# Kernel tuning notes

Measured on AMD Instinct MI355X. Metric: run time of the kernel, lower is better.

The kernel has to match this reference:

```python
import jax, jax.numpy as jnp
import numpy as np

B, T, DIM = 2, 2048, 2048
N_HEADS, N_KV_HEADS = 16, 4
HEAD_DIM = DIM // N_HEADS  # 128
N_REP = N_HEADS // N_KV_HEADS  # 4
ROPE_THETA = 10000.0


def setup_inputs() -> dict:
    key = jax.random.key(0)
    ks = jax.random.split(key, 5)
    x = jax.random.normal(ks[0], (B, T, DIM), dtype=jnp.float32)
    # RoPE tables (equivalent to complex freqs_cis = exp(i * t * inv_freq))
    inv_freq = 1.0 / (ROPE_THETA ** (np.arange(0, HEAD_DIM, 2, dtype=np.float32) / HEAD_DIM))
    t = np.arange(T, dtype=np.float32)
    ang = np.outer(t, inv_freq)  # (T, HEAD_DIM//2)
    freqs_cos = jnp.asarray(np.cos(ang), dtype=jnp.float32)
    freqs_sin = jnp.asarray(np.sin(ang), dtype=jnp.float32)
    s = 0.02
    wq = jax.random.normal(ks[1], (DIM, N_HEADS * HEAD_DIM), dtype=jnp.float32) * s
    wk = jax.random.normal(ks[2], (DIM, N_KV_HEADS * HEAD_DIM), dtype=jnp.float32) * s
    wv = jax.random.normal(ks[3], (DIM, N_KV_HEADS * HEAD_DIM), dtype=jnp.float32) * s
    wo = jax.random.normal(ks[4], (N_HEADS * HEAD_DIM, DIM), dtype=jnp.float32) * s
    return {"x": x, "freqs_cos": freqs_cos, "freqs_sin": freqs_sin,
            "wq": wq, "wk": wk, "wv": wv, "wo": wo}


def _apply_rope(t, cos, sin):
    # t: (B, H, T, hd); cos/sin: (T, hd//2); interleaved pairs like view_as_complex
    tr = t[..., 0::2]
    ti = t[..., 1::2]
    c = cos[None, None, :, :]
    s = sin[None, None, :, :]
    out_r = tr * c - ti * s
    out_i = tr * s + ti * c
    return jnp.stack([out_r, out_i], axis=-1).reshape(t.shape)


def reference(x, freqs_cos, freqs_sin, wq, wk, wv, wo):
    Bb, Tt, C = x.shape
    q = (x @ wq).reshape(Bb, Tt, N_HEADS, HEAD_DIM).transpose(0, 2, 1, 3)      # (B,H,T,hd)
    k = (x @ wk).reshape(Bb, Tt, N_KV_HEADS, HEAD_DIM).transpose(0, 2, 1, 3)   # (B,KV,T,hd)
    v = (x @ wv).reshape(Bb, Tt, N_KV_HEADS, HEAD_DIM).transpose(0, 2, 1, 3)
    q = _apply_rope(q, freqs_cos[:Tt], freqs_sin[:Tt])
    k = _apply_rope(k, freqs_cos[:Tt], freqs_sin[:Tt])
    # GQA repeat_kv
    k = jnp.repeat(k, N_REP, axis=1)  # (B,H,T,hd)
    v = jnp.repeat(v, N_REP, axis=1)
    scale = 1.0 / jnp.sqrt(jnp.float32(HEAD_DIM))
    scores = jnp.einsum("bhqd,bhkd->bhqk", q, k) * scale
    causal = jnp.tril(jnp.ones((Tt, Tt), dtype=bool))
    scores = jnp.where(causal[None, None], scores, jnp.float32(-jnp.inf))
    attn = jax.nn.softmax(scores, axis=-1)
    out = jnp.einsum("bhqk,bhkd->bhqd", attn, v)          # (B,H,T,hd)
    out = out.transpose(0, 2, 1, 3).reshape(Bb, Tt, C)
    return out @ wo
```

## Files before the change

kernel.cpp:

```cpp
#include <hip/hip_runtime.h>
#include <hip/hip_bf16.h>

#define SEQT 2048
#define NH 16
#define HD 128

typedef __bf16 bf16;
typedef __bf16 bf16x4 __attribute__((ext_vector_type(4)));
typedef __bf16 bf16x8 __attribute__((ext_vector_type(8)));
typedef float f32x4 __attribute__((ext_vector_type(4)));
typedef float f32x16 __attribute__((ext_vector_type(16)));

__device__ inline void glds16(const bf16* g, bf16* l) {
  __builtin_amdgcn_global_load_lds(
      (const __attribute__((address_space(1))) unsigned int*)g,
      (__attribute__((address_space(3))) unsigned int*)l, 16, 0, 0);
}

__device__ inline unsigned int cvtpk(float a, float b) {
  unsigned int d;
  asm("v_cvt_pk_bf16_f32 %0, %1, %2" : "=v"(d) : "v"(a), "v"(b));
  return d;
}

__global__ __launch_bounds__(256) void k_convert(const float* __restrict__ in,
                                                 bf16* __restrict__ out, int n8) {
  int i = blockIdx.x * 256 + threadIdx.x;
  if (i >= n8) return;
  const float4* p = (const float4*)in + (size_t)i * 2;
  float4 a = p[0], b = p[1];
  bf16x8 o;
  o[0] = (bf16)a.x; o[1] = (bf16)a.y; o[2] = (bf16)a.z; o[3] = (bf16)a.w;
  o[4] = (bf16)b.x; o[5] = (bf16)b.y; o[6] = (bf16)b.z; o[7] = (bf16)b.w;
  *((bf16x8*)out + i) = o;
}

__global__ __launch_bounds__(256) void k_transpose(const float* __restrict__ in,
                                                   bf16* __restrict__ out, int R, int C) {
  __shared__ float tile[32][33];
  int c0 = blockIdx.x * 32, r0 = blockIdx.y * 32;
  int tx = threadIdx.x, ty = threadIdx.y;
#pragma unroll
  for (int i = 0; i < 4; i++)
    tile[ty + i * 8][tx] = in[(size_t)(r0 + ty + i * 8) * C + c0 + tx];
  __syncthreads();
#pragma unroll
  for (int i = 0; i < 4; i++) {
    int r = ty + i * 8;
    out[(size_t)(c0 + r) * R + r0 + tx] = (bf16)tile[tx][r];
  }
}

template <typename OutT>
__global__ __launch_bounds__(256) void k_gemm(const bf16* __restrict__ A,
                                              const bf16* __restrict__ Bt,
                                              OutT* __restrict__ C,
                                              int M, int N, int K, int ldc) {
  __shared__ bf16 Al[128 * 32];
  __shared__ bf16 Bl[128 * 32];
  int tid = threadIdx.x;
  int m0 = blockIdx.y * 128, n0 = blockIdx.x * 128;
  int wid = tid >> 6, lane = tid & 63;
  int wr = (wid >> 1) * 64, wc = (wid & 1) * 64;
  int lr = lane & 15, lk = (lane >> 4) * 8;
  f32x4 acc[4][4] = {};

  for (int k0 = 0; k0 < K; k0 += 32) {
#pragma unroll
    for (int i = 0; i < 2; i++) {
      int idx = i * 256 + tid;
      int r = idx >> 2, kc = (idx & 3) * 8;
      glds16(A + (size_t)(m0 + r) * K + k0 + kc, Al + idx * 8);
      glds16(Bt + (size_t)(n0 + r) * K + k0 + kc, Bl + idx * 8);
    }
    __syncthreads();
    bf16x8 af[4], bfr[4];
#pragma unroll
    for (int mi = 0; mi < 4; mi++) af[mi] = *(const bf16x8*)&Al[(wr + mi * 16 + lr) * 32 + lk];
#pragma unroll
    for (int ni = 0; ni < 4; ni++) bfr[ni] = *(const bf16x8*)&Bl[(wc + ni * 16 + lr) * 32 + lk];
#pragma unroll
    for (int mi = 0; mi < 4; mi++)
#pragma unroll
      for (int ni = 0; ni < 4; ni++)
        acc[mi][ni] = __builtin_amdgcn_mfma_f32_16x16x32_bf16(af[mi], bfr[ni], acc[mi][ni], 0, 0, 0);
    __syncthreads();
  }

  int rbase = m0 + wr + ((lane >> 4) << 2);
#pragma unroll
  for (int mi = 0; mi < 4; mi++)
#pragma unroll
    for (int ni = 0; ni < 4; ni++)
#pragma unroll
      for (int r = 0; r < 4; r++) {
        int row = rbase + mi * 16 + r;
        int col = n0 + wc + ni * 16 + lr;
        C[(size_t)row * ldc + col] = (OutT)acc[mi][ni][r];
      }
}

__global__ __launch_bounds__(256) void k_rope(bf16* __restrict__ qkv,
                                              const float* __restrict__ fcos,
                                              const float* __restrict__ fsin) {
  int gid = blockIdx.x * 256 + threadIdx.x;
  int row = gid / 1280;
  int p = gid % 1280;
  int head = p >> 6;
  int dp = p & 63;
  int t = row & (SEQT - 1);
  int colbase = head < NH ? head * HD : NH * HD + (head - NH) * HD;
  bf16* ptr = qkv + (size_t)row * 3072 + colbase + dp * 2;
  float a = (float)ptr[0], b = (float)ptr[1];
  float c = fcos[t * 64 + dp], s = fsin[t * 64 + dp];
  ptr[0] = (bf16)(a * c - b * s);
  ptr[1] = (bf16)(a * s + b * c);
}

__global__ __launch_bounds__(256, 2) void k_attn(const bf16* __restrict__ qkv,
                                                 bf16* __restrict__ attout) {
  __shared__ bf16 Kl[2][8192];
  __shared__ bf16 Vt[2][128][72];
  __shared__ float Tabs[4][4][32];
  int bid = blockIdx.x;
  int qt = 31 - (bid >> 5);
  int bh = bid & 31;
  int b = bh >> 4, h = bh & 15, kvh = h >> 2;
  int tid = threadIdx.x, wid = tid >> 6, lane = tid & 63;
  int grp = wid >> 1, wq = wid & 1;
  int li = lane & 31, hi = lane >> 5;
  int q0 = qt * 64;
  int qmin = q0 + wq * 32, qmax = qmin + 31;
  int qlane = qmin + li;
  const float C1 = 0.12751744979927212f;

  const bf16* kgbase = qkv + (size_t)b * SEQT * 3072 + 2048 + kvh * HD;
  const bf16* vgbase = kgbase + 512;

  bf16x8 qf[8];
  {
    const bf16* qb = qkv + (size_t)(b * SEQT + qlane) * 3072 + h * HD + hi * 8;
#pragma unroll
    for (int ks = 0; ks < 8; ks++) qf[ks] = *(const bf16x8*)(qb + ks * 16);
  }

  float mrun = -INFINITY, lpart = 0.f;
  f32x16 o0 = {}, o1 = {}, o2 = {}, o3 = {};
  int nkt = qt + 1;

  int g = (lane >> 4) & 3;
  int lr = lane & 15;
  int kq4 = (wid * 4 + g) * 4;
  int dc = lr * 8;
  int xr = (lr & 7) << 3;
  int kvw = kq4 ^ xr;

  bf16x8 vr0, vr1, vr2, vr3;

#pragma unroll
  for (int r = 0; r < 4; r++) {
    int ci = r * 256 + tid;
    int row = ci >> 4;
    int sl = (ci & 15) ^ (row & 15);
    glds16(kgbase + (size_t)row * 3072 + sl * 8, &Kl[0][ci * 8]);
  }
  {
    const bf16* vrow = vgbase + (size_t)kq4 * 3072 + dc;
    vr0 = *(const bf16x8*)(vrow);
    vr1 = *(const bf16x8*)(vrow + 3072);
    vr2 = *(const bf16x8*)(vrow + 6144);
    vr3 = *(const bf16x8*)(vrow + 9216);
  }

  for (int kt = 0; kt < nkt; kt++) {
    int cur = kt & 1;
    int kv0 = kt * 64;
    asm volatile("s_waitcnt vmcnt(0)" ::: "memory");

#pragma unroll
    for (int j = 0; j < 8; j++) {
      bf16x4 w;
      w[0] = vr0[j]; w[1] = vr1[j]; w[2] = vr2[j]; w[3] = vr3[j];
      *(bf16x4*)&Vt[cur][dc + j][kvw] = w;
    }

    asm volatile("s_waitcnt lgkmcnt(0)" ::: "memory");
    __builtin_amdgcn_sched_barrier(0);
    __builtin_amdgcn_s_barrier();
    __builtin_amdgcn_sched_barrier(0);

    if (kt + 1 < nkt) {
      int kv1 = kv0 + 64;
      bf16* kdst = &Kl[cur ^ 1][0];
#pragma unroll
      for (int r = 0; r < 4; r++) {
        int ci = r * 256 + tid;
        int row = ci >> 4;
        int sl = (ci & 15) ^ (row & 15);
        glds16(kgbase + (size_t)(kv1 + row) * 3072 + sl * 8, kdst + ci * 8);
      }
      const bf16* vrow = vgbase + (size_t)(kv1 + kq4) * 3072 + dc;
      vr0 = *(const bf16x8*)(vrow);
      vr1 = *(const bf16x8*)(vrow + 3072);
      vr2 = *(const bf16x8*)(vrow + 6144);
      vr3 = *(const bf16x8*)(vrow + 9216);
    }

    if (grp == cur && kv0 <= qmax) {
      f32x16 s0 = {}, s1 = {};
      const char* kb0 = (const char*)&Kl[cur][0] + li * 256;
      __builtin_amdgcn_s_setprio(1);
#pragma unroll
      for (int ks = 0; ks < 8; ks++) {
        int off = ((ks * 2 + hi) ^ (li & 15)) << 4;
        bf16x8 kf0 = *(const bf16x8*)(kb0 + off);
        bf16x8 kf1 = *(const bf16x8*)(kb0 + 8192 + off);
        s0 = __builtin_amdgcn_mfma_f32_32x32x16_bf16(kf0, qf[ks], s0, 0, 0, 0);
        s1 = __builtin_amdgcn_mfma_f32_32x32x16_bf16(kf1, qf[ks], s1, 0, 0, 0);
      }
      __builtin_amdgcn_s_setprio(0);

      if (kv0 + 63 > qmin) {
        int base0 = kv0 + 4 * hi - qlane;
#pragma unroll
        for (int r = 0; r < 16; r++) {
          int off = (r & 3) + 8 * (r >> 2);
          if (base0 + off > 0) s0[r] = -INFINITY;
          if (base0 + 32 + off > 0) s1[r] = -INFINITY;
        }
      }

      float pm = s0[0];
#pragma unroll
      for (int r = 1; r < 16; r++) pm = fmaxf(pm, s0[r]);
#pragma unroll
      for (int r = 0; r < 16; r++) pm = fmaxf(pm, s1[r]);
      pm = fmaxf(pm, __shfl_xor(pm, 32));

      if (!__all(pm - mrun <= 62.0f)) {
        float mnew = fmaxf(mrun, pm);
        float alpha = exp2f((mrun - mnew) * C1);
        mrun = mnew;
        lpart *= alpha;
        Tabs[0][wid][li] = alpha;
        asm volatile("s_waitcnt lgkmcnt(0)" ::: "memory");
        f32x4 a0 = *(const f32x4*)&Tabs[0][wid][4 * hi];
        f32x4 a1 = *(const f32x4*)&Tabs[0][wid][4 * hi + 8];
        f32x4 a2 = *(const f32x4*)&Tabs[0][wid][4 * hi + 16];
        f32x4 a3 = *(const f32x4*)&Tabs[0][wid][4 * hi + 24];
#define RESC_RR(rr, av)                                            \
  _Pragma("unroll") for (int i = 0; i < 4; i++) {                  \
    float f = av[i];                                               \
    o0[rr * 4 + i] *= f; o1[rr * 4 + i] *= f;                      \
    o2[rr * 4 + i] *= f; o3[rr * 4 + i] *= f;                      \
  }
        RESC_RR(0, a0) RESC_RR(1, a1) RESC_RR(2, a2) RESC_RR(3, a3)
#undef RESC_RR
      }

      float mC = mrun * C1;
      float rs = 0.f;
#pragma unroll
      for (int r = 0; r < 16; r++) {
        float p = exp2f(fmaf(s0[r], C1, -mC));
        s0[r] = p; rs += p;
      }
#pragma unroll
      for (int r = 0; r < 16; r++) {
        float p = exp2f(fmaf(s1[r], C1, -mC));
        s1[r] = p; rs += p;
      }
      lpart += rs;

      union U4 { unsigned int u[4]; bf16x8 v; };
      U4 pa0, pa1, pa2, pa3;
      {
        unsigned int e0 = cvtpk(s0[0], s0[1]), e1 = cvtpk(s0[2], s0[3]);
        unsigned int e2 = cvtpk(s0[4], s0[5]), e3 = cvtpk(s0[6], s0[7]);
        unsigned int e4 = cvtpk(s0[8], s0[9]), e5 = cvtpk(s0[10], s0[11]);
        unsigned int e6 = cvtpk(s0[12], s0[13]), e7 = cvtpk(s0[14], s0[15]);
        unsigned int t0 = __shfl_xor(e0, 32), t1 = __shfl_xor(e1, 32);
        unsigned int t2 = __shfl_xor(e2, 32), t3 = __shfl_xor(e3, 32);
        unsigned int t4 = __shfl_xor(e4, 32), t5 = __shfl_xor(e5, 32);
        unsigned int t6 = __shfl_xor(e6, 32), t7 = __shfl_xor(e7, 32);
        pa0.u[0] = hi ? t2 : e0;  pa0.u[1] = hi ? t3 : e1;
        pa0.u[2] = hi ? e2 : t0;  pa0.u[3] = hi ? e3 : t1;
        pa1.u[0] = hi ? t6 : e4;  pa1.u[1] = hi ? t7 : e5;
        pa1.u[2] = hi ? e6 : t4;  pa1.u[3] = hi ? e7 : t5;
        unsigned int f0 = cvtpk(s1[0], s1[1]), f1 = cvtpk(s1[2], s1[3]);
        unsigned int f2 = cvtpk(s1[4], s1[5]), f3 = cvtpk(s1[6], s1[7]);
        unsigned int f4 = cvtpk(s1[8], s1[9]), f5 = cvtpk(s1[10], s1[11]);
        unsigned int f6 = cvtpk(s1[12], s1[13]), f7 = cvtpk(s1[14], s1[15]);
        unsigned int u0 = __shfl_xor(f0, 32), u1 = __shfl_xor(f1, 32);
        unsigned int u2 = __shfl_xor(f2, 32), u3 = __shfl_xor(f3, 32);
        unsigned int u4 = __shfl_xor(f4, 32), u5 = __shfl_xor(f5, 32);
        unsigned int u6 = __shfl_xor(f6, 32), u7 = __shfl_xor(f7, 32);
        pa2.u[0] = hi ? u2 : f0;  pa2.u[1] = hi ? u3 : f1;
        pa2.u[2] = hi ? f2 : u0;  pa2.u[3] = hi ? f3 : u1;
        pa3.u[0] = hi ? u6 : f4;  pa3.u[1] = hi ? u7 : f5;
        pa3.u[2] = hi ? f6 : u4;  pa3.u[3] = hi ? f7 : u5;
      }

      __builtin_amdgcn_s_setprio(1);
#define PV_DB(OACC, DB)                                                      \
  {                                                                          \
    int d = DB * 32 + li;                                                    \
    int xv = ((d >> 3) & 7) << 3;                                            \
    bf16x8 vb0 = *(const bf16x8*)&Vt[cur][d][(hi * 8) ^ xv];                 \
    bf16x8 vb1 = *(const bf16x8*)&Vt[cur][d][(16 + hi * 8) ^ xv];            \
    bf16x8 vb2 = *(const bf16x8*)&Vt[cur][d][(32 + hi * 8) ^ xv];            \
    bf16x8 vb3 = *(const bf16x8*)&Vt[cur][d][(48 + hi * 8) ^ xv];            \
    OACC = __builtin_amdgcn_mfma_f32_32x32x16_bf16(pa0.v, vb0, OACC, 0, 0, 0); \
    OACC = __builtin_amdgcn_mfma_f32_32x32x16_bf16(pa1.v, vb1, OACC, 0, 0, 0); \
    OACC = __builtin_amdgcn_mfma_f32_32x32x16_bf16(pa2.v, vb2, OACC, 0, 0, 0); \
    OACC = __builtin_amdgcn_mfma_f32_32x32x16_bf16(pa3.v, vb3, OACC, 0, 0, 0); \
  }
      PV_DB(o0, 0) PV_DB(o1, 1) PV_DB(o2, 2) PV_DB(o3, 3)
#undef PV_DB
      __builtin_amdgcn_s_setprio(0);
    }
  }

  lpart += __shfl_xor(lpart, 32);
  Tabs[0][wid][li] = mrun;
  Tabs[1][wid][li] = lpart;
  asm volatile("s_waitcnt lgkmcnt(0)" ::: "memory");
  __builtin_amdgcn_s_barrier();
  int peer = wid ^ 2;
  float mP = Tabs[0][peer][li], lP = Tabs[1][peer][li];
  float mS = fmaxf(mrun, mP);
  float fMe = exp2f((mrun - mS) * C1);
  float fPe = exp2f((mP - mS) * C1);
  float lTot = lpart * fMe + lP * fPe;
  Tabs[2][wid][li] = fMe;
  Tabs[3][wid][li] = 1.f / lTot;
  asm volatile("s_waitcnt lgkmcnt(0)" ::: "memory");
  __builtin_amdgcn_s_barrier();
  f32x4 Fv0 = *(const f32x4*)&Tabs[2][wid][4 * hi];
  f32x4 Fv1 = *(const f32x4*)&Tabs[2][wid][4 * hi + 8];
  f32x4 Fv2 = *(const f32x4*)&Tabs[2][wid][4 * hi + 16];
  f32x4 Fv3 = *(const f32x4*)&Tabs[2][wid][4 * hi + 24];
  f32x4 Iv0 = *(const f32x4*)&Tabs[3][wid][4 * hi];
  f32x4 Iv1 = *(const f32x4*)&Tabs[3][wid][4 * hi + 8];
  f32x4 Iv2 = *(const f32x4*)&Tabs[3][wid][4 * hi + 16];
  f32x4 Iv3 = *(const f32x4*)&Tabs[3][wid][4 * hi + 24];

  float* X = (float*)&Kl[0][0];
  float* Xb = X + (wid & 1) * 4096;
  if (grp == 1) {
#define XW_RR(OACC, DB, rr, Fv)                                              \
  _Pragma("unroll") for (int i = 0; i < 4; i++)                              \
    Xb[(4 * hi + 8 * rr + i) * 128 + DB * 32 + li] = OACC[rr * 4 + i] * Fv[i];
#define XW_DB(OACC, DB) XW_RR(OACC, DB, 0, Fv0) XW_RR(OACC, DB, 1, Fv1) \
                        XW_RR(OACC, DB, 2, Fv2) XW_RR(OACC, DB, 3, Fv3)
    XW_DB(o0, 0) XW_DB(o1, 1) XW_DB(o2, 2) XW_DB(o3, 3)
#undef XW_DB
#undef XW_RR
  }
  asm volatile("s_waitcnt lgkmcnt(0)" ::: "memory");
  __builtin_amdgcn_s_barrier();
  if (grp == 0) {
#define XR_RR(OACC, DB, rr, Fv)                                              \
  _Pragma("unroll") for (int i = 0; i < 4; i++)                              \
    OACC[rr * 4 + i] = OACC[rr * 4 + i] * Fv[i] +                            \
        Xb[(4 * hi + 8 * rr + i) * 128 + DB * 32 + li];
#define XR_DB(OACC, DB) XR_RR(OACC, DB, 0, Fv0) XR_RR(OACC, DB, 1, Fv1) \
                        XR_RR(OACC, DB, 2, Fv2) XR_RR(OACC, DB, 3, Fv3)
    XR_DB(o0, 0) XR_DB(o1, 1) XR_DB(o2, 2) XR_DB(o3, 3)
#undef XR_DB
#undef XR_RR
    size_t obase = (size_t)(b * SEQT) * 2048 + h * HD;
#define STORE_RR(rr, lv)                                                     \
  _Pragma("unroll") for (int i = 0; i < 4; i++) {                            \
    int q = qmin + 4 * hi + 8 * rr + i;                                      \
    size_t rowb = obase + (size_t)q * 2048 + li;                             \
    attout[rowb + 0]  = (bf16)(o0[rr * 4 + i] * lv[i]);                      \
    attout[rowb + 32] = (bf16)(o1[rr * 4 + i] * lv[i]);                      \
    attout[rowb + 64] = (bf16)(o2[rr * 4 + i] * lv[i]);                      \
    attout[rowb + 96] = (bf16)(o3[rr * 4 + i] * lv[i]);                      \
  }
    STORE_RR(0, Iv0) STORE_RR(1, Iv1) STORE_RR(2, Iv2) STORE_RR(3, Iv3)
#undef STORE_RR
  }
}

extern "C" void kernel_launch(void* const* d_in, const int* in_sizes, int n_in,
                              void* d_out, int out_size, void* d_ws, size_t ws_size,
                              hipStream_t stream) {
  const float* x    = (const float*)d_in[0];
  const float* fcos = (const float*)d_in[1];
  const float* fsin = (const float*)d_in[2];
  const float* wq   = (const float*)d_in[3];
  const float* wk   = (const float*)d_in[4];
  const float* wv   = (const float*)d_in[5];
  const float* wo   = (const float*)d_in[6];
  float* out = (float*)d_out;

  char* ws = (char*)d_ws;
  bf16* XB  = (bf16*)ws;
  bf16* W   = (bf16*)(ws + 16777216);
  bf16* QKV = (bf16*)(ws + 16777216 + 12582912);

  dim3 tb(32, 8);
  k_transpose<<<dim3(64, 64), tb, 0, stream>>>(wq, W, 2048, 2048);
  k_transpose<<<dim3(16, 64), tb, 0, stream>>>(wk, W + 2048 * 2048, 2048, 512);
  k_transpose<<<dim3(16, 64), tb, 0, stream>>>(wv, W + 2560 * 2048, 2048, 512);
  k_convert<<<4096, 256, 0, stream>>>(x, XB, 1048576);
  k_gemm<bf16><<<dim3(24, 32), 256, 0, stream>>>(XB, W, QKV, 4096, 3072, 2048, 3072);
  k_rope<<<20480, 256, 0, stream>>>(QKV, fcos, fsin);
  k_attn<<<1024, 256, 0, stream>>>(QKV, XB);
  k_transpose<<<dim3(64, 64), tb, 0, stream>>>(wo, W, 2048, 2048);
  k_gemm<float><<<dim3(16, 32), 256, 0, stream>>>(XB, W, out, 4096, 2048, 2048, 2048);
}
```

Baseline: 248.9 us.

## Split KV tile across wave pairs in attention, single V buffer, fuse QKV transposes

Attention work is restructured so both wave pairs process every KV tile, each taking one 32-key half, instead of alternating whole tiles between the pairs. V is now held in a single LDS buffer and a second barrier is added at the end of each iteration. This lowers LDS use and raises the occupancy hint from 2 to 3 blocks per CU. The three weight transpose launches for wq, wk and wv are merged into one kernel to cut launch overhead. The trade-off is an extra barrier per KV tile and less time for V loads to overlap with compute.

New measurement: 337.8 us. 35.7% more time.

```diff
diff --git a/kernel.cpp b/kernel.cpp
--- a/kernel.cpp
+++ b/kernel.cpp
@@ -48,6 +48,35 @@
   for (int i = 0; i < 4; i++) {
     int r = ty + i * 8;
     out[(size_t)(c0 + r) * R + r0 + tx] = (bf16)tile[tx][r];
+  }
+}
+
+__global__ __launch_bounds__(256) void k_transpose3(const float* __restrict__ wq,
+                                                    const float* __restrict__ wk,
+                                                    const float* __restrict__ wv,
+                                                    bf16* __restrict__ W) {
+  __shared__ float tile[32][33];
+  int bx = blockIdx.x;
+  const float* src;
+  bf16* dst;
+  int C;
+  if (bx < 64) {
+    src = wq; dst = W; C = 2048;
+  } else if (bx < 80) {
+    src = wk; dst = W + 2048 * 2048; C = 512; bx -= 64;
+  } else {
+    src = wv; dst = W + 2560 * 2048; C = 512; bx -= 80;
+  }
+  int c0 = bx * 32, r0 = blockIdx.y * 32;
+  int tx = threadIdx.x, ty = threadIdx.y;
+#pragma unroll
+  for (int i = 0; i < 4; i++)
+    tile[ty + i * 8][tx] = src[(size_t)(r0 + ty + i * 8) * C + c0 + tx];
+  __syncthreads();
+#pragma unroll
+  for (int i = 0; i < 4; i++) {
+    int r = ty + i * 8;
+    dst[(size_t)(c0 + r) * 2048 + r0 + tx] = (bf16)tile[tx][r];
   }
 }
 
@@ -117,17 +146,17 @@
   ptr[1] = (bf16)(a * s + b * c);
 }
 
-__global__ __launch_bounds__(256, 2) void k_attn(const bf16* __restrict__ qkv,
+__global__ __launch_bounds__(256, 3) void k_attn(const bf16* __restrict__ qkv,
                                                  bf16* __restrict__ attout) {
   __shared__ bf16 Kl[2][8192];
-  __shared__ bf16 Vt[2][128][72];
+  __shared__ bf16 Vt[128][72];
   __shared__ float Tabs[4][4][32];
   int bid = blockIdx.x;
   int qt = 31 - (bid >> 5);
   int bh = bid & 31;
   int b = bh >> 4, h = bh & 15, kvh = h >> 2;
   int tid = threadIdx.x, wid = tid >> 6, lane = tid & 63;
-  int grp = wid >> 1, wq = wid & 1;
+  int kvhalf = wid >> 1, wq = wid & 1;
   int li = lane & 31, hi = lane >> 5;
   int q0 = qt * 64;
   int qmin = q0 + wq * 32, qmax = qmin + 31;
@@ -147,6 +176,7 @@
   float mrun = -INFINITY, lpart = 0.f;
   f32x16 o0 = {}, o1 = {}, o2 = {}, o3 = {};
   int nkt = qt + 1;
+  int kvbase = 32 * kvhalf;
 
   int g = (lane >> 4) & 3;
   int lr = lane & 15;
@@ -181,13 +211,8 @@
     for (int j = 0; j < 8; j++) {
       bf16x4 w;
       w[0] = vr0[j]; w[1] = vr1[j]; w[2] = vr2[j]; w[3] = vr3[j];
-      *(bf16x4*)&Vt[cur][dc + j][kvw] = w;
+      *(bf16x4*)&Vt[dc + j][kvw] = w;
     }
-
-    asm volatile("s_waitcnt lgkmcnt(0)" ::: "memory");
-    __builtin_amdgcn_sched_barrier(0);
-    __builtin_amdgcn_s_barrier();
-    __builtin_amdgcn_sched_barrier(0);
 
     if (kt + 1 < nkt) {
       int kv1 = kv0 + 64;
@@ -206,35 +231,35 @@
       vr3 = *(const bf16x8*)(vrow + 9216);
     }
 
-    if (grp == cur && kv0 <= qmax) {
-      f32x16 s0 = {}, s1 = {};
-      const char* kb0 = (const char*)&Kl[cur][0] + li * 256;
+    asm volatile("s_waitcnt lgkmcnt(0)" ::: "memory");
+    __builtin_amdgcn_sched_barrier(0);
+    __builtin_amdgcn_s_barrier();
+    __builtin_amdgcn_sched_barrier(0);
+
+    if (kv0 + kvbase <= qmax) {
+      f32x16 s0 = {};
+      const char* kb0 = (const char*)&Kl[cur][0] + kvhalf * 8192 + li * 256;
       __builtin_amdgcn_s_setprio(1);
 #pragma unroll
       for (int ks = 0; ks < 8; ks++) {
         int off = ((ks * 2 + hi) ^ (li & 15)) << 4;
         bf16x8 kf0 = *(const bf16x8*)(kb0 + off);
-        bf16x8 kf1 = *(const bf16x8*)(kb0 + 8192 + off);
         s0 = __builtin_amdgcn_mfma_f32_32x32x16_bf16(kf0, qf[ks], s0, 0, 0, 0);
-        s1 = __builtin_amdgcn_mfma_f32_32x32x16_bf16(kf1, qf[ks], s1, 0, 0, 0);
       }
       __builtin_amdgcn_s_setprio(0);
 
-      if (kv0 + 63 > qmin) {
-        int base0 = kv0 + 4 * hi - qlane;
+      if (kv0 + kvbase + 31 > qmin) {
+        int base0 = kv0 + kvbase + 4 * hi - qlane;
 #pragma unroll
         for (int r = 0; r < 16; r++) {
           int off = (r & 3) + 8 * (r >> 2);
           if (base0 + off > 0) s0[r] = -INFINITY;
-          if (base0 + 32 + off > 0) s1[r] = -INFINITY;
         }
       }
 
       float pm = s0[0];
 #pragma unroll
       for (int r = 1; r < 16; r++) pm = fmaxf(pm, s0[r]);
-#pragma unroll
-      for (int r = 0; r < 16; r++) pm = fmaxf(pm, s1[r]);
       pm = fmaxf(pm, __shfl_xor(pm, 32));
 
       if (!__all(pm - mrun <= 62.0f)) {
@@ -265,15 +290,10 @@
         float p = exp2f(fmaf(s0[r], C1, -mC));
         s0[r] = p; rs += p;
       }
-#pragma unroll
-      for (int r = 0; r < 16; r++) {
-        float p = exp2f(fmaf(s1[r], C1, -mC));
-        s1[r] = p; rs += p;
-      }
       lpart += rs;
 
       union U4 { unsigned int u[4]; bf16x8 v; };
-      U4 pa0, pa1, pa2, pa3;
+      U4 pa0, pa1;
       {
         unsigned int e0 = cvtpk(s0[0], s0[1]), e1 = cvtpk(s0[2], s0[3]);
         unsigned int e2 = cvtpk(s0[4], s0[5]), e3 = cvtpk(s0[6], s0[7]);
@@ -287,18 +307,6 @@
         pa0.u[2] = hi ? e2 : t0;  pa0.u[3] = hi ? e3 : t1;
         pa1.u[0] = hi ? t6 : e4;  pa1.u[1] = hi ? t7 : e5;
         pa1.u[2] = hi ? e6 : t4;  pa1.u[3] = hi ? e7 : t5;
-        unsigned int f0 = cvtpk(s1[0], s1[1]), f1 = cvtpk(s1[2], s1[3]);
-        unsigned int f2 = cvtpk(s1[4], s1[5]), f3 = cvtpk(s1[6], s1[7]);
-        unsigned int f4 = cvtpk(s1[8], s1[9]), f5 = cvtpk(s1[10], s1[11]);
-        unsigned int f6 = cvtpk(s1[12], s1[13]), f7 = cvtpk(s1[14], s1[15]);
-        unsigned int u0 = __shfl_xor(f0, 32), u1 = __shfl_xor(f1, 32);
-        unsigned int u2 = __shfl_xor(f2, 32), u3 = __shfl_xor(f3, 32);
-        unsigned int u4 = __shfl_xor(f4, 32), u5 = __shfl_xor(f5, 32);
-        unsigned int u6 = __shfl_xor(f6, 32), u7 = __shfl_xor(f7, 32);
-        pa2.u[0] = hi ? u2 : f0;  pa2.u[1] = hi ? u3 : f1;
-        pa2.u[2] = hi ? f2 : u0;  pa2.u[3] = hi ? f3 : u1;
-        pa3.u[0] = hi ? u6 : f4;  pa3.u[1] = hi ? u7 : f5;
-        pa3.u[2] = hi ? f6 : u4;  pa3.u[3] = hi ? f7 : u5;
       }
 
       __builtin_amdgcn_s_setprio(1);
@@ -306,19 +314,19 @@
   {                                                                          \
     int d = DB * 32 + li;                                                    \
     int xv = ((d >> 3) & 7) << 3;                                            \
-    bf16x8 vb0 = *(const bf16x8*)&Vt[cur][d][(hi * 8) ^ xv];                 \
-    bf16x8 vb1 = *(const bf16x8*)&Vt[cur][d][(16 + hi * 8) ^ xv];            \
-    bf16x8 vb2 = *(const bf16x8*)&Vt[cur][d][(32 + hi * 8) ^ xv];            \
-    bf16x8 vb3 = *(const bf16x8*)&Vt[cur][d][(48 + hi * 8) ^ xv];            \
+    bf16x8 vb0 = *(const bf16x8*)&Vt[d][(kvbase + hi * 8) ^ xv];             \
+    bf16x8 vb1 = *(const bf16x8*)&Vt[d][(kvbase + 16 + hi * 8) ^ xv];        \
     OACC = __builtin_amdgcn_mfma_f32_32x32x16_bf16(pa0.v, vb0, OACC, 0, 0, 0); \
     OACC = __builtin_amdgcn_mfma_f32_32x32x16_bf16(pa1.v, vb1, OACC, 0, 0, 0); \
-    OACC = __builtin_amdgcn_mfma_f32_32x32x16_bf16(pa2.v, vb2, OACC, 0, 0, 0); \
-    OACC = __builtin_amdgcn_mfma_f32_32x32x16_bf16(pa3.v, vb3, OACC, 0, 0, 0); \
   }
       PV_DB(o0, 0) PV_DB(o1, 1) PV_DB(o2, 2) PV_DB(o3, 3)
 #undef PV_DB
       __builtin_amdgcn_s_setprio(0);
     }
+
+    __builtin_amdgcn_sched_barrier(0);
+    __builtin_amdgcn_s_barrier();
+    __builtin_amdgcn_sched_barrier(0);
   }
 
   lpart += __shfl_xor(lpart, 32);
@@ -347,7 +355,7 @@
 
   float* X = (float*)&Kl[0][0];
   float* Xb = X + (wid & 1) * 4096;
-  if (grp == 1) {
+  if (kvhalf == 1) {
 #define XW_RR(OACC, DB, rr, Fv)                                              \
   _Pragma("unroll") for (int i = 0; i < 4; i++)                              \
     Xb[(4 * hi + 8 * rr + i) * 128 + DB * 32 + li] = OACC[rr * 4 + i] * Fv[i];
@@ -359,7 +367,7 @@
   }
   asm volatile("s_waitcnt lgkmcnt(0)" ::: "memory");
   __builtin_amdgcn_s_barrier();
-  if (grp == 0) {
+  if (kvhalf == 0) {
 #define XR_RR(OACC, DB, rr, Fv)                                              \
   _Pragma("unroll") for (int i = 0; i < 4; i++)                              \
     OACC[rr * 4 + i] = OACC[rr * 4 + i] * Fv[i] +                            \
@@ -402,9 +410,7 @@
   bf16* QKV = (bf16*)(ws + 16777216 + 12582912);
 
   dim3 tb(32, 8);
-  k_transpose<<<dim3(64, 64), tb, 0, stream>>>(wq, W, 2048, 2048);
-  k_transpose<<<dim3(16, 64), tb, 0, stream>>>(wk, W + 2048 * 2048, 2048, 512);
-  k_transpose<<<dim3(16, 64), tb, 0, stream>>>(wv, W + 2560 * 2048, 2048, 512);
+  k_transpose3<<<dim3(96, 64), tb, 0, stream>>>(wq, wk, wv, W);
   k_convert<<<4096, 256, 0, stream>>>(x, XB, 1048576);
   k_gemm<bf16><<<dim3(24, 32), 256, 0, stream>>>(XB, W, QKV, 4096, 3072, 2048, 3072);
   k_rope<<<20480, 256, 0, stream>>>(QKV, fcos, fsin);
```
